# Kernel optimization log

Measured on AMD Instinct MI355X. Metric: run time of the kernel, lower is better.

## Reference

```python
import jax, jax.numpy as jnp
import numpy as np

B, N = 2, 65536
OUT_FEATS = (64, 128, 256)
RES = (64, 32, 16)
EPS = 1e-8


def _grid_sample_border(feat, uv):
    # feat: (B,C,H,W); uv: (B,Np,2) normalized to [-1,1], align_corners=True,
    # bilinear, padding_mode='border' (matches F.grid_sample semantics).
    Bb, C, H, W = feat.shape
    f = jnp.transpose(feat, (0, 2, 3, 1))  # (B,H,W,C)
    ix = jnp.clip((uv[..., 0] + 1.0) * 0.5 * (W - 1), 0.0, W - 1)
    iy = jnp.clip((uv[..., 1] + 1.0) * 0.5 * (H - 1), 0.0, H - 1)
    x0 = jnp.floor(ix); y0 = jnp.floor(iy)
    wx = (ix - x0)[..., None]; wy = (iy - y0)[..., None]
    x0i = x0.astype(jnp.int32); y0i = y0.astype(jnp.int32)
    x1i = jnp.minimum(x0i + 1, W - 1); y1i = jnp.minimum(y0i + 1, H - 1)
    b = jnp.arange(Bb)[:, None]
    v00 = f[b, y0i, x0i]; v01 = f[b, y0i, x1i]
    v10 = f[b, y1i, x0i]; v11 = f[b, y1i, x1i]
    return (v00 * (1 - wx) * (1 - wy) + v01 * wx * (1 - wy)
            + v10 * (1 - wx) * wy + v11 * wx * wy)  # (B,Np,C)


def _projection(img_feat, init_pc, extrinsic, intrinsic):
    homo = jnp.concatenate([init_pc, jnp.ones_like(init_pc[..., :1])], axis=-1)  # (B,N,4)
    P = jnp.einsum('bij,bjk->bik', intrinsic, extrinsic)  # (B,3,4)
    pln = jnp.einsum('bik,bnk->bni', P, homo)  # (B,N,3)
    X, Y, Z = pln[..., 0], pln[..., 1], pln[..., 2]
    uv = jnp.stack([-X / Z, Y / Z], axis=-1)  # sign = -1 since is_srn_proj=False
    return _grid_sample_border(img_feat, uv)


def _adain(pc_feat, img_feat, fcw, fcb):
    mu = jnp.mean(pc_feat, axis=-1, keepdims=True)
    var = jnp.var(pc_feat, axis=-1, ddof=1, keepdims=True)  # torch unbiased var
    pcn = (pc_feat - mu) / jnp.sqrt(var + EPS)
    im_mean = jnp.mean(img_feat, axis=(2, 3))  # (B,C)
    im_var = jnp.var(img_feat.reshape(img_feat.shape[0], img_feat.shape[1], -1), axis=2, ddof=1)
    out = (pcn + im_mean[:, None]) * jnp.sqrt(im_var[:, None] + EPS)
    return out @ fcw + fcb


def setup_inputs() -> dict:
    key = jax.random.key(0)
    ks = iter(jax.random.split(key, 64))
    inp = {}
    inp['init_pc'] = jax.random.uniform(next(ks), (B, N, 3), minval=-1.0, maxval=1.0)
    # extrinsic = [I | t] with t = (0,0,4) plus tiny noise -> Z in ~[3,5], safe division
    ex = jnp.concatenate([jnp.eye(3), jnp.array([[0.0], [0.0], [4.0]])], axis=1)
    inp['extrinsic'] = jnp.broadcast_to(ex, (B, 3, 4)) + 0.01 * jax.random.normal(next(ks), (B, 3, 4))
    intr = jnp.diag(jnp.array([1.2, 1.2, 1.0]))
    inp['intrinsic'] = jnp.broadcast_to(intr, (B, 3, 3)) + 0.01 * jax.random.normal(next(ks), (B, 3, 3))
    for i, (c, r) in enumerate(zip(OUT_FEATS, RES)):
        inp[f'img_feat{i}'] = jax.random.normal(next(ks), (B, c, r, r), dtype=jnp.float32)
    dim = 3
    for i, c in enumerate(OUT_FEATS):
        inp[f'w1_{i}'] = 0.05 * jax.random.normal(next(ks), (dim, c))
        inp[f'b1_{i}'] = jnp.zeros((c,))
        inp[f'w2_{i}'] = 0.05 * jax.random.normal(next(ks), (c, c))
        inp[f'b2_{i}'] = jnp.zeros((c,))
        inp[f'fcw_{i}'] = 0.05 * jax.random.normal(next(ks), (c, c))
        inp[f'fcb_{i}'] = jnp.zeros((c,))
        dim = c
    return inp


def reference(img_feat0, img_feat1, img_feat2, init_pc, extrinsic, intrinsic,
              w1_0, b1_0, w2_0, b2_0, fcw_0, fcb_0,
              w1_1, b1_1, w2_1, b2_1, fcw_1, fcb_1,
              w1_2, b1_2, w2_2, b2_2, fcw_2, fcb_2):
    imgs = [img_feat0, img_feat1, img_feat2]
    blocks = [(w1_0, b1_0, w2_0, b2_0, fcw_0, fcb_0),
              (w1_1, b1_1, w2_1, b2_1, fcw_1, fcb_1),
              (w1_2, b1_2, w2_2, b2_2, fcw_2, fcb_2)]
    pc_feats = []
    feat = init_pc
    encoded = []
    for (w1, b1, w2, b2, _, _) in blocks:  # fixed 3-layer stack
        feat = jax.nn.relu(jax.nn.relu(feat @ w1 + b1) @ w2 + b2)
        encoded.append(feat)
    for pcf, img, (_, _, _, _, fcw, fcb) in zip(encoded, imgs, blocks):
        pc_feats.append(_adain(pcf, img, fcw, fcb))
    for img in imgs:
        pc_feats.append(_projection(img, init_pc, extrinsic, intrinsic))
    pc_feats.append(init_pc)
    return jnp.concatenate(pc_feats, axis=-1)  # (B, N, 2*(64+128+256)+3) = (B,N,899)
```

## Files before the change

### kernel.cpp

```cpp
#include <hip/hip_runtime.h>
#include <hip/hip_bf16.h>

typedef __hip_bfloat16 bf16;
typedef unsigned short u16;
typedef unsigned int u32;
typedef __attribute__((ext_vector_type(8))) short s8b;
typedef __attribute__((ext_vector_type(16))) float f32x16;

#define EPSF 1e-8f

__device__ __align__(16) u16 g_wpack[256000];
__device__ __align__(16) u16 g_fcpack[344064];
__device__ float g_bias[896];
__device__ float g_fcS[896];
__device__ float g_fcC[896];
__device__ float g_T0[2 * 64 * 64 * 64];
__device__ float g_T1[2 * 128 * 32 * 32];
__device__ float g_T2[2 * 256 * 16 * 16];

__device__ __forceinline__ float ldf(const void* p, size_t i, int f32v) {
  return f32v ? ((const float*)p)[i] : __bfloat162float(((const bf16*)p)[i]);
}
template <bool F32>
__device__ __forceinline__ float ld(const void* p, size_t i) {
  if constexpr (F32) return ((const float*)p)[i];
  else return __bfloat162float(((const bf16*)p)[i]);
}
__device__ __forceinline__ void stf(void* p, size_t i, float v, int f32v) {
  if (f32v) ((float*)p)[i] = v;
  else ((bf16*)p)[i] = __float2bfloat16(v);
}
__device__ __forceinline__ int detect_f32(const void* extr) {
  float v = ((const float*)extr)[0];
  return (fabsf(v - 1.0f) < 0.25f) ? 1 : 0;
}

__device__ __forceinline__ void splitbf(float v, u16& h, u16& l) {
  bf16 hb = __float2bfloat16(v);
  float hf = __bfloat162float(hb);
  bf16 lb = __float2bfloat16(v - hf);
  h = __builtin_bit_cast(u16, hb);
  l = __builtin_bit_cast(u16, lb);
}
__device__ __forceinline__ float bfjoin(u16 h, u16 l) {
  return __uint_as_float((u32)h << 16) + __uint_as_float((u32)l << 16);
}

__device__ __forceinline__ u16* xaddr(u16* base, int row, int col) {
  int byte = (row << 9) + (col << 1);
  byte ^= (row & 7) << 4;
  return (u16*)((char*)base + byte);
}
__device__ __forceinline__ const u16* xaddrc(const u16* base, int row, int col) {
  int byte = (row << 9) + (col << 1);
  byte ^= (row & 7) << 4;
  return (const u16*)((const char*)base + byte);
}

__device__ __forceinline__ f32x16 MFMA32(s8b a, s8b b, f32x16 c) {
  return __builtin_amdgcn_mfma_f32_32x32x16_bf16(a, b, c, 0, 0, 0);
}

template <bool F32>
__device__ void stats_body(const void* img0, const void* img1, const void* img2,
                           const void* intr, const void* extr,
                           float* wsf, float* red) {
  int bid = blockIdx.x;
  if (bid >= 896) {
    int b = bid - 896;
    int t = threadIdx.x;
    if (t < 12) {
      int r = t >> 2, c = t & 3;
      float acc = 0.f;
      for (int k = 0; k < 3; ++k)
        acc += ld<F32>(intr, b * 9 + r * 3 + k) * ld<F32>(extr, b * 12 + k * 4 + c);
      wsf[b * 12 + r * 4 + c] = acc;
    }
    return;
  }
  const void* src; size_t base; int HW, outidx;
  if (bid < 128) {
    int b = bid >> 6, c = bid & 63;
    src = img0; base = (size_t)(b * 64 + c) * 4096; HW = 4096;
    outidx = 32 + b * 64 + c;
  } else if (bid < 384) {
    int t = bid - 128; int b = t >> 7, c = t & 127;
    src = img1; base = (size_t)(b * 128 + c) * 1024; HW = 1024;
    outidx = 32 + 128 + b * 128 + c;
  } else {
    int t = bid - 384; int b = t >> 8, c = t & 255;
    src = img2; base = (size_t)(b * 256 + c) * 256; HW = 256;
    outidx = 32 + 384 + b * 256 + c;
  }
  float s1 = 0.f, s2 = 0.f;
  for (int i = threadIdx.x; i < HW; i += 256) {
    float v = ld<F32>(src, base + i);
    s1 += v; s2 += v * v;
  }
  for (int off = 32; off; off >>= 1) {
    s1 += __shfl_xor(s1, off);
    s2 += __shfl_xor(s2, off);
  }
  int wid = threadIdx.x >> 6, lane = threadIdx.x & 63;
  if (lane == 0) { red[wid] = s1; red[4 + wid] = s2; }
  __syncthreads();
  if (threadIdx.x == 0) {
    float S1 = red[0] + red[1] + red[2] + red[3];
    float S2 = red[4] + red[5] + red[6] + red[7];
    float mu = S1 / (float)HW;
    float var = (S2 - (float)HW * mu * mu) / (float)(HW - 1);
    var = fmaxf(var, 0.f);
    wsf[outidx] = mu;
    wsf[outidx + 896] = sqrtf(var + EPSF);
  }
}

__global__ __launch_bounds__(256) void prep1(
    const void* img0, const void* img1, const void* img2,
    const void* intr, const void* extr,
    const void* w1_0, const void* w2_0, const void* w1_1, const void* w2_1,
    const void* w1_2, const void* w2_2,
    const void* b1_0, const void* b2_0, const void* b1_1, const void* b2_1,
    const void* b1_2, const void* b2_2,
    float* wsf) {
  __shared__ float red[8];
  const int f32v = detect_f32(extr);
  int bid = blockIdx.x;
  int tid = threadIdx.x;

  if (bid < 898) {
    if (f32v) stats_body<true>(img0, img1, img2, intr, extr, wsf, red);
    else      stats_body<false>(img0, img1, img2, intr, extr, wsf, red);
    return;
  }
  if (bid < 4482) {
    const void* src; float* dst; int C, R, i0;
    if (bid < 2946)       { src = img0; dst = g_T0; C = 64;  R = 64; i0 = (bid - 898) * 256; }
    else if (bid < 3970)  { src = img1; dst = g_T1; C = 128; R = 32; i0 = (bid - 2946) * 256; }
    else                  { src = img2; dst = g_T2; C = 256; R = 16; i0 = (bid - 3970) * 256; }
    int i = i0 + tid;
    int x = i % R; int t = i / R;
    int y = t % R; t /= R;
    int c = t % C; int b = t / C;
    dst[((size_t)(b * R + y) * R + x) * C + c] = ldf(src, i, f32v);
    return;
  }
  if (bid < 4607) {
    int chunk = (bid - 4482) * 4 + (tid >> 6);
    int lane = tid & 63;
    if (chunk < 500) {
      const int nch[6]   = {4, 16, 32, 64, 128, 256};
      const int cbase[6] = {0, 4, 20, 52, 116, 244};
      const int couts[6] = {64, 64, 128, 128, 256, 256};
      const int kreal[6] = {3, 64, 64, 128, 128, 256};
      const void* wp[6] = {w1_0, w2_0, w1_1, w2_1, w1_2, w2_2};
      int layer = 5;
      for (int s = 0; s < 5; ++s) if (chunk < cbase[s + 1]) { layer = s; break; }
      int ci = chunk - cbase[layer];
      int COUT = couts[layer], KR = kreal[layer];
      int STR = COUT >> 5;
      int ks = ci / (STR * 2);
      int rem = ci % (STR * 2);
      int nt = rem >> 1, split = rem & 1;
      const void* W = wp[layer];
      s8b sv;
#pragma unroll
      for (int j = 0; j < 8; ++j) {
        int k = ks * 16 + 8 * (lane >> 5) + j;
        int c = nt * 32 + (lane & 31);
        float v = (k < KR) ? ldf(W, (size_t)k * COUT + c, f32v) : 0.f;
        u16 h, l; splitbf(v, h, l);
        sv[j] = (short)(split == 0 ? h : l);
      }
      *(s8b*)((char*)g_wpack + (size_t)chunk * 1024 + lane * 16) = sv;
    }
    return;
  }
  {
    int t = (bid - 4607) * 256 + tid;
    if (t < 896) {
      const int off[7] = {0, 64, 128, 256, 384, 640, 896};
      const void* bp[6] = {b1_0, b2_0, b1_1, b2_1, b1_2, b2_2};
      int seg = 0;
      while (seg < 5 && t >= off[seg + 1]) ++seg;
      g_bias[t] = ldf(bp[seg], t - off[seg], f32v);
    }
  }
}

__global__ __launch_bounds__(256) void prep2(
    const void* extr,
    const void* fcw_0, const void* fcw_1, const void* fcw_2,
    const void* fcb_0, const void* fcb_1, const void* fcb_2,
    const float* wsf) {
  const int f32v = detect_f32(extr);
  int bid = blockIdx.x;
  int tid = threadIdx.x;
  if (bid < 168) {
    int chunk = bid * 4 + (tid >> 6);
    int lane = tid & 63;
    int bb = chunk / 336;
    int ci = chunk % 336;
    int C, COUT, loff; const void* W;
    if (ci < 16)      { C = 64;  COUT = 64;  loff = 0;   W = fcw_0; }
    else if (ci < 80) { C = 128; COUT = 128; loff = 128; W = fcw_1; ci -= 16; }
    else              { C = 256; COUT = 256; loff = 384; W = fcw_2; ci -= 80; }
    int STR = COUT >> 5;
    int ks = ci / (STR * 2);
    int rem = ci % (STR * 2);
    int nt = rem >> 1, split = rem & 1;
    const float* sig = wsf + 928 + loff + bb * C;
    s8b sv;
#pragma unroll
    for (int j = 0; j < 8; ++j) {
      int k = ks * 16 + 8 * (lane >> 5) + j;
      int c = nt * 32 + (lane & 31);
      float v = sig[k] * ldf(W, (size_t)k * COUT + c, f32v);
      u16 h, l; splitbf(v, h, l);
      sv[j] = (short)(split == 0 ? h : l);
    }
    *(s8b*)((char*)g_fcpack + (size_t)chunk * 1024 + lane * 16) = sv;
    return;
  }
  {
    int idx = bid - 168;
    if (idx >= 6) return;
    int bb = idx / 3, layer = idx % 3;
    int C, colbase, loff; const void* W; const void* fb;
    if (layer == 0)      { C = 64;  colbase = 0;   loff = 0;   W = fcw_0; fb = fcb_0; }
    else if (layer == 1) { C = 128; colbase = 64;  loff = 128; W = fcw_1; fb = fcb_1; }
    else                 { C = 256; colbase = 192; loff = 384; W = fcw_2; fb = fcb_2; }
    int j = tid;
    if (j >= C) return;
    const float* sig = wsf + 928 + loff + bb * C;
    const float* mean = wsf + 32 + loff + bb * C;
    float S = 0.f, Cv = 0.f;
    for (int c = 0; c < C; ++c) {
      float w = sig[c] * ldf(W, (size_t)c * C + j, f32v);
      S += w;
      Cv += mean[c] * w;
    }
    Cv += ldf(fb, j, f32v);
    g_fcS[bb * 448 + colbase + j] = S;
    g_fcC[bb * 448 + colbase + j] = Cv;
  }
}

template <int KS, int COUT, int NTW, bool HASBIAS>
__device__ __forceinline__ void mm32(
    const u16* Xh_, const u16* Xl_, const char* wlane,
    const float* biasp, int nt0, int lane, f32x16* acc) {
#pragma unroll
  for (int n = 0; n < NTW; ++n) {
    float bv = HASBIAS ? biasp[(nt0 + n) * 32 + (lane & 31)] : 0.f;
#pragma unroll
    for (int q = 0; q < 16; ++q) acc[n][q] = bv;
  }
  const int rowA = lane & 31;
  const int acol = (lane >> 5) * 8;
#pragma unroll
  for (int ks = 0; ks < KS; ++ks) {
    s8b ah = *(const s8b*)xaddrc(Xh_, rowA, ks * 16 + acol);
    s8b al = *(const s8b*)xaddrc(Xl_, rowA, ks * 16 + acol);
#pragma unroll
    for (int n = 0; n < NTW; ++n) {
      const char* ch = wlane + (size_t)((ks * (COUT / 32) + nt0 + n) * 2) * 1024;
      s8b bh = *(const s8b*)(ch);
      s8b bl = *(const s8b*)(ch + 1024);
      acc[n] = MFMA32(ah, bh, acc[n]);
      acc[n] = MFMA32(ah, bl, acc[n]);
      acc[n] = MFMA32(al, bh, acc[n]);
    }
  }
}

template <int COUT>
__device__ __forceinline__ void strip_assign(int wid, int& nt0, int& active) {
  if constexpr (COUT == 64)      { nt0 = (wid & 1);  active = (wid < 2); }
  else if constexpr (COUT == 128){ nt0 = wid;        active = 1; }
  else                           { nt0 = wid * 2;    active = 1; }
}

template <int KS, int COUT>
__device__ __forceinline__ void dense32(u16* Xh_, u16* Xl_,
                                        int wbyte, int bbase, int tid) {
  constexpr int NTW = (COUT == 256) ? 2 : 1;
  int lane = tid & 63, wid = tid >> 6;
  int nt0, active;
  strip_assign<COUT>(wid, nt0, active);
  f32x16 acc[NTW];
  if (active)
    mm32<KS, COUT, NTW, true>(Xh_, Xl_,
        (const char*)g_wpack + wbyte + lane * 16, g_bias + bbase, nt0, lane, acc);
  __syncthreads();
  if (active) {
    int g = lane >> 5;
#pragma unroll
    for (int n = 0; n < NTW; ++n) {
      int col = (nt0 + n) * 32 + (lane & 31);
#pragma unroll
      for (int q = 0; q < 16; ++q) {
        int row = (q & 3) + 8 * (q >> 2) + 4 * g;
        float v = fmaxf(acc[n][q], 0.f);
        u16 h, l; splitbf(v, h, l);
        *xaddr(Xh_, row, col) = h;
        *xaddr(Xl_, row, col) = l;
      }
    }
  }
  __syncthreads();
}

template <int C>
__device__ __forceinline__ void musig(const u16* Xh_, const u16* Xl_,
                                      int lane, float& mu, float& rs) {
  int row = lane & 31;
  int c0 = (lane >> 5) * (C / 2);
  float s1 = 0.f, s2 = 0.f;
#pragma unroll
  for (int k = 0; k < C / 2; k += 8) {
    s8b h = *(const s8b*)xaddrc(Xh_, row, c0 + k);
    s8b l = *(const s8b*)xaddrc(Xl_, row, c0 + k);
#pragma unroll
    for (int i = 0; i < 8; ++i) {
      float f = bfjoin((u16)h[i], (u16)l[i]);
      s1 += f; s2 += f * f;
    }
  }
  s1 += __shfl_xor(s1, 32);
  s2 += __shfl_xor(s2, 32);
  mu = s1 / (float)C;
  float var = (s2 - (float)C * mu * mu) / (float)(C - 1);
  var = fmaxf(var, 0.f);
  rs = 1.0f / sqrtf(var + EPSF);
}

template <int KS, int COUT>
__device__ __forceinline__ void fc32(const u16* Xh_, const u16* Xl_,
    int fcbyte, int scbase, float mu, float rs,
    void* out, u32 R0, int colbase, int f32v, int tid) {
  constexpr int NTW = (COUT == 256) ? 2 : 1;
  int lane = tid & 63, wid = tid >> 6;
  int nt0, active;
  strip_assign<COUT>(wid, nt0, active);
  if (!active) return;
  f32x16 acc[NTW];
  mm32<KS, COUT, NTW, false>(Xh_, Xl_,
      (const char*)g_fcpack + fcbyte + lane * 16, nullptr, nt0, lane, acc);
  float Sv[NTW], Cv[NTW];
  u32 gcol[NTW];
#pragma unroll
  for (int n = 0; n < NTW; ++n) {
    int lc = (nt0 + n) * 32 + (lane & 31);
    Sv[n] = g_fcS[scbase + lc];
    Cv[n] = g_fcC[scbase + lc];
    gcol[n] = colbase + lc;
  }
  int g = lane >> 5;
  if (f32v) {
#pragma unroll
    for (int q = 0; q < 16; ++q) {
      int row = (q & 3) + 8 * (q >> 2) + 4 * g;
      float m = __shfl(mu, row);
      float r = __shfl(rs, row);
      u32 grow = (R0 + row) * 899u;
#pragma unroll
      for (int n = 0; n < NTW; ++n)
        ((float*)out)[grow + gcol[n]] = r * (acc[n][q] - m * Sv[n]) + Cv[n];
    }
  } else {
#pragma unroll
    for (int q = 0; q < 16; ++q) {
      int row = (q & 3) + 8 * (q >> 2) + 4 * g;
      float m = __shfl(mu, row);
      float r = __shfl(rs, row);
      u32 grow = (R0 + row) * 899u;
#pragma unroll
      for (int n = 0; n < NTW; ++n)
        ((bf16*)out)[grow + gcol[n]] =
            __float2bfloat16(r * (acc[n][q] - m * Sv[n]) + Cv[n]);
    }
  }
}

template <int C, int R>
__device__ __forceinline__ void sample(
    const float* T, float u, float v, int b, int lane,
    void* out, u32 obase, int f32v) {
  constexpr int J = C / 64;
  float ix = fminf(fmaxf((u + 1.f) * 0.5f * (float)(R - 1), 0.f), (float)(R - 1));
  float iy = fminf(fmaxf((v + 1.f) * 0.5f * (float)(R - 1), 0.f), (float)(R - 1));
  float x0f = floorf(ix), y0f = floorf(iy);
  float wx = ix - x0f, wy = iy - y0f;
  int x0 = (int)x0f, y0 = (int)y0f;
  int x1 = min(x0 + 1, R - 1), y1 = min(y0 + 1, R - 1);
  float w00 = (1.f - wx) * (1.f - wy), w01 = wx * (1.f - wy);
  float w10 = (1.f - wx) * wy,         w11 = wx * wy;
  const float* T00 = T + (size_t)((b * R + y0) * R + x0) * C;
  const float* T01 = T + (size_t)((b * R + y0) * R + x1) * C;
  const float* T10 = T + (size_t)((b * R + y1) * R + x0) * C;
  const float* T11 = T + (size_t)((b * R + y1) * R + x1) * C;
  float sv[J];
#pragma unroll
  for (int j = 0; j < J; ++j) {
    int c = lane + 64 * j;
    sv[j] = T00[c] * w00 + T01[c] * w01 + T10[c] * w10 + T11[c] * w11;
  }
  if (f32v) {
#pragma unroll
    for (int j = 0; j < J; ++j)
      ((float*)out)[obase + lane + 64 * j] = sv[j];
  } else {
#pragma unroll
    for (int j = 0; j < J; ++j)
      ((bf16*)out)[obase + lane + 64 * j] = __float2bfloat16(sv[j]);
  }
}

__device__ void projection(const void* init_pc, const float* wsf, void* out,
                           u32 R0, int b, int f32v, int tid) {
  int lane = tid & 63, wid = tid >> 6;
  float Pm[12];
#pragma unroll
  for (int i = 0; i < 12; ++i) Pm[i] = wsf[b * 12 + i];
  for (int p = 0; p < 8; ++p) {
    u32 n = R0 + wid * 8 + p;
    float px = ldf(init_pc, (size_t)n * 3 + 0, f32v);
    float py = ldf(init_pc, (size_t)n * 3 + 1, f32v);
    float pz = ldf(init_pc, (size_t)n * 3 + 2, f32v);
    float X = Pm[0] * px + Pm[1] * py + Pm[2] * pz + Pm[3];
    float Y = Pm[4] * px + Pm[5] * py + Pm[6] * pz + Pm[7];
    float Z = Pm[8] * px + Pm[9] * py + Pm[10] * pz + Pm[11];
    float u = -X / Z, vv = Y / Z;
    u32 rowb = n * 899u;
    sample<64, 64>(g_T0, u, vv, b, lane, out, rowb + 448, f32v);
    sample<128, 32>(g_T1, u, vv, b, lane, out, rowb + 512, f32v);
    sample<256, 16>(g_T2, u, vv, b, lane, out, rowb + 640, f32v);
    if (lane < 3) {
      float pv = (lane == 0) ? px : (lane == 1) ? py : pz;
      stf(out, rowb + 896 + lane, pv, f32v);
    }
  }
}

__global__ __launch_bounds__(256, 5) void pce_main(
    const void* init_pc, const void* extr, const float* wsf, void* out) {
  __shared__ u16 Xh[8192];
  __shared__ u16 Xl[8192];
  const int f32v = detect_f32(extr);
  const int tid = threadIdx.x;
  const int lane = tid & 63;
  const u32 R0 = blockIdx.x * 32;
  const int b = (int)(R0 >> 16);

  for (int i = tid; i < 512; i += 256) {
    int r = i >> 4, c = i & 15;
    *xaddr(Xh, r, c) = 0;
    *xaddr(Xl, r, c) = 0;
  }
  __syncthreads();
  if (tid < 96) {
    int r = tid / 3, c = tid % 3;
    float v = ldf(init_pc, (size_t)(R0 + r) * 3 + c, f32v);
    u16 h, l; splitbf(v, h, l);
    *xaddr(Xh, r, c) = h;
    *xaddr(Xl, r, c) = l;
  }
  __syncthreads();

  dense32<1, 64>(Xh, Xl, 0, 0, tid);
  dense32<4, 64>(Xh, Xl, 4096, 64, tid);
  { float mu, rs; musig<64>(Xh, Xl, lane, mu, rs);
    fc32<4, 64>(Xh, Xl, b * 344064 + 0, b * 448 + 0, mu, rs, out, R0, 0, f32v, tid); }

  dense32<4, 128>(Xh, Xl, 20480, 128, tid);
  dense32<8, 128>(Xh, Xl, 53248, 256, tid);
  { float mu, rs; musig<128>(Xh, Xl, lane, mu, rs);
    fc32<8, 128>(Xh, Xl, b * 344064 + 16384, b * 448 + 64, mu, rs, out, R0, 64, f32v, tid); }

  dense32<8, 256>(Xh, Xl, 118784, 384, tid);
  dense32<16, 256>(Xh, Xl, 249856, 640, tid);
  { float mu, rs; musig<256>(Xh, Xl, lane, mu, rs);
    fc32<16, 256>(Xh, Xl, b * 344064 + 81920, b * 448 + 192, mu, rs, out, R0, 192, f32v, tid); }

  projection(init_pc, wsf, out, R0, b, f32v, tid);
}

extern "C" void kernel_launch(void* const* d_in, const int* in_sizes, int n_in,
                              void* d_out, int out_size, void* d_ws, size_t ws_size,
                              hipStream_t stream) {
  const void* init_pc = d_in[0];
  const void* extr    = d_in[1];
  const void* intr    = d_in[2];
  const void* img0    = d_in[3];
  const void* img1    = d_in[4];
  const void* img2    = d_in[5];
  const void* w1_0 = d_in[6],  *b1_0 = d_in[7];
  const void* w2_0 = d_in[8],  *b2_0 = d_in[9];
  const void* fcw_0 = d_in[10], *fcb_0 = d_in[11];
  const void* w1_1 = d_in[12], *b1_1 = d_in[13];
  const void* w2_1 = d_in[14], *b2_1 = d_in[15];
  const void* fcw_1 = d_in[16], *fcb_1 = d_in[17];
  const void* w1_2 = d_in[18], *b1_2 = d_in[19];
  const void* w2_2 = d_in[20], *b2_2 = d_in[21];
  const void* fcw_2 = d_in[22], *fcb_2 = d_in[23];

  float* wsf = (float*)d_ws;

  prep1<<<4611, 256, 0, stream>>>(
      img0, img1, img2, intr, extr,
      w1_0, w2_0, w1_1, w2_1, w1_2, w2_2,
      b1_0, b2_0, b1_1, b2_1, b1_2, b2_2, wsf);
  prep2<<<174, 256, 0, stream>>>(
      extr, fcw_0, fcw_1, fcw_2, fcb_0, fcb_1, fcb_2, wsf);
  pce_main<<<4096, 256, 0, stream>>>(init_pc, extr, wsf, d_out);
}
```

Before: 900.9 us.

## Stage output rows in shared memory for coalesced stores; tile image transpose

The main kernel keeps the three FC accumulators live, then assembles 8 full 899-wide output rows at a time in shared memory (FC results, sampled projections, raw points). It writes them out as contiguous, coalesced non-temporal stores, packing bf16 pairs into 32-bit words. The goal is to replace the scattered strided per-column global writes. The image NHWC transpose in prep1 now goes through a padded shared tile, one block per (batch,row) plane, so both reads and writes are coalesced. The costs are higher register pressure (occupancy hint lowered to 3), extra barriers, and per-element division in the store loop.

Measured after the change: 809.5 us. 1.11x faster.

```diff
diff --git a/kernel.cpp b/kernel.cpp
--- a/kernel.cpp
+++ b/kernel.cpp
@@ -26,10 +26,6 @@
   if constexpr (F32) return ((const float*)p)[i];
   else return __bfloat162float(((const bf16*)p)[i]);
 }
-__device__ __forceinline__ void stf(void* p, size_t i, float v, int f32v) {
-  if (f32v) ((float*)p)[i] = v;
-  else ((bf16*)p)[i] = __float2bfloat16(v);
-}
 __device__ __forceinline__ int detect_f32(const void* extr) {
   float v = ((const float*)extr)[0];
   return (fabsf(v - 1.0f) < 0.25f) ? 1 : 0;
@@ -44,6 +40,9 @@
 }
 __device__ __forceinline__ float bfjoin(u16 h, u16 l) {
   return __uint_as_float((u32)h << 16) + __uint_as_float((u32)l << 16);
+}
+__device__ __forceinline__ u16 f2bfu(float v) {
+  return __builtin_bit_cast(u16, __float2bfloat16(v));
 }
 
 __device__ __forceinline__ u16* xaddr(u16* base, int row, int col) {
@@ -124,6 +123,7 @@
     const void* b1_2, const void* b2_2,
     float* wsf) {
   __shared__ float red[8];
+  __shared__ float tl[4352];
   const int f32v = detect_f32(extr);
   int bid = blockIdx.x;
   int tid = threadIdx.x;
@@ -133,23 +133,28 @@
     else      stats_body<false>(img0, img1, img2, intr, extr, wsf, red);
     return;
   }
-  if (bid < 4482) {
-    const void* src; float* dst; int C, R, i0;
-    if (bid < 2946)       { src = img0; dst = g_T0; C = 64;  R = 64; i0 = (bid - 898) * 256; }
-    else if (bid < 3970)  { src = img1; dst = g_T1; C = 128; R = 32; i0 = (bid - 2946) * 256; }
-    else                  { src = img2; dst = g_T2; C = 256; R = 16; i0 = (bid - 3970) * 256; }
-    int i = i0 + tid;
-    int x = i % R; int t = i / R;
-    int y = t % R; t /= R;
-    int c = t % C; int b = t / C;
-    dst[((size_t)(b * R + y) * R + x) * C + c] = ldf(src, i, f32v);
+  if (bid < 1122) {
+    int pl = bid - 898;
+    const void* src; float* dst; int C, R, rsh, csh, b, y;
+    if (pl < 128)      { src = img0; dst = g_T0; C = 64;  R = 64; rsh = 6; csh = 6; b = pl >> 6; y = pl & 63; }
+    else if (pl < 192) { src = img1; dst = g_T1; C = 128; R = 32; rsh = 5; csh = 7; int q = pl - 128; b = q >> 5; y = q & 31; }
+    else               { src = img2; dst = g_T2; C = 256; R = 16; rsh = 4; csh = 8; int q = pl - 192; b = q >> 4; y = q & 15; }
+    int CR = C * R;
+    for (int i = tid; i < CR; i += 256) {
+      int c = i >> rsh, x = i & (R - 1);
+      tl[c * (R + 1) + x] = ldf(src, ((size_t)(b * C + c) * R + y) * R + x, f32v);
+    }
+    __syncthreads();
+    for (int i = tid; i < CR; i += 256) {
+      int x = i >> csh, c = i & (C - 1);
+      dst[((size_t)(b * R + y) * R + x) * C + c] = tl[c * (R + 1) + x];
+    }
     return;
   }
-  if (bid < 4607) {
-    int chunk = (bid - 4482) * 4 + (tid >> 6);
+  if (bid < 1247) {
+    int chunk = (bid - 1122) * 4 + (tid >> 6);
     int lane = tid & 63;
     if (chunk < 500) {
-      const int nch[6]   = {4, 16, 32, 64, 128, 256};
       const int cbase[6] = {0, 4, 20, 52, 116, 244};
       const int couts[6] = {64, 64, 128, 128, 256, 256};
       const int kreal[6] = {3, 64, 64, 128, 128, 256};
@@ -177,7 +182,7 @@
     return;
   }
   {
-    int t = (bid - 4607) * 256 + tid;
+    int t = (bid - 1247) * 256 + tid;
     if (t < 896) {
       const int off[7] = {0, 64, 128, 256, 384, 640, 896};
       const void* bp[6] = {b1_0, b2_0, b1_1, b2_1, b1_2, b2_2};
@@ -274,20 +279,15 @@
   }
 }
 
-template <int COUT>
-__device__ __forceinline__ void strip_assign(int wid, int& nt0, int& active) {
-  if constexpr (COUT == 64)      { nt0 = (wid & 1);  active = (wid < 2); }
-  else if constexpr (COUT == 128){ nt0 = wid;        active = 1; }
-  else                           { nt0 = wid * 2;    active = 1; }
-}
-
 template <int KS, int COUT>
 __device__ __forceinline__ void dense32(u16* Xh_, u16* Xl_,
                                         int wbyte, int bbase, int tid) {
   constexpr int NTW = (COUT == 256) ? 2 : 1;
   int lane = tid & 63, wid = tid >> 6;
   int nt0, active;
-  strip_assign<COUT>(wid, nt0, active);
+  if constexpr (COUT == 64)      { nt0 = (wid & 1);  active = (wid < 2); }
+  else if constexpr (COUT == 128){ nt0 = wid;        active = 1; }
+  else                           { nt0 = wid * 2;    active = 1; }
   f32x16 acc[NTW];
   if (active)
     mm32<KS, COUT, NTW, true>(Xh_, Xl_,
@@ -335,58 +335,9 @@
   rs = 1.0f / sqrtf(var + EPSF);
 }
 
-template <int KS, int COUT>
-__device__ __forceinline__ void fc32(const u16* Xh_, const u16* Xl_,
-    int fcbyte, int scbase, float mu, float rs,
-    void* out, u32 R0, int colbase, int f32v, int tid) {
-  constexpr int NTW = (COUT == 256) ? 2 : 1;
-  int lane = tid & 63, wid = tid >> 6;
-  int nt0, active;
-  strip_assign<COUT>(wid, nt0, active);
-  if (!active) return;
-  f32x16 acc[NTW];
-  mm32<KS, COUT, NTW, false>(Xh_, Xl_,
-      (const char*)g_fcpack + fcbyte + lane * 16, nullptr, nt0, lane, acc);
-  float Sv[NTW], Cv[NTW];
-  u32 gcol[NTW];
-#pragma unroll
-  for (int n = 0; n < NTW; ++n) {
-    int lc = (nt0 + n) * 32 + (lane & 31);
-    Sv[n] = g_fcS[scbase + lc];
-    Cv[n] = g_fcC[scbase + lc];
-    gcol[n] = colbase + lc;
-  }
-  int g = lane >> 5;
-  if (f32v) {
-#pragma unroll
-    for (int q = 0; q < 16; ++q) {
-      int row = (q & 3) + 8 * (q >> 2) + 4 * g;
-      float m = __shfl(mu, row);
-      float r = __shfl(rs, row);
-      u32 grow = (R0 + row) * 899u;
-#pragma unroll
-      for (int n = 0; n < NTW; ++n)
-        ((float*)out)[grow + gcol[n]] = r * (acc[n][q] - m * Sv[n]) + Cv[n];
-    }
-  } else {
-#pragma unroll
-    for (int q = 0; q < 16; ++q) {
-      int row = (q & 3) + 8 * (q >> 2) + 4 * g;
-      float m = __shfl(mu, row);
-      float r = __shfl(rs, row);
-      u32 grow = (R0 + row) * 899u;
-#pragma unroll
-      for (int n = 0; n < NTW; ++n)
-        ((bf16*)out)[grow + gcol[n]] =
-            __float2bfloat16(r * (acc[n][q] - m * Sv[n]) + Cv[n]);
-    }
-  }
-}
-
 template <int C, int R>
-__device__ __forceinline__ void sample(
-    const float* T, float u, float v, int b, int lane,
-    void* out, u32 obase, int f32v) {
+__device__ __forceinline__ void sample_stg(
+    const float* T, float u, float v, int b, int lane, float* stg) {
   constexpr int J = C / 64;
   float ix = fminf(fmaxf((u + 1.f) * 0.5f * (float)(R - 1), 0.f), (float)(R - 1));
   float iy = fminf(fmaxf((v + 1.f) * 0.5f * (float)(R - 1), 0.f), (float)(R - 1));
@@ -400,56 +351,24 @@
   const float* T01 = T + (size_t)((b * R + y0) * R + x1) * C;
   const float* T10 = T + (size_t)((b * R + y1) * R + x0) * C;
   const float* T11 = T + (size_t)((b * R + y1) * R + x1) * C;
-  float sv[J];
 #pragma unroll
   for (int j = 0; j < J; ++j) {
     int c = lane + 64 * j;
-    sv[j] = T00[c] * w00 + T01[c] * w01 + T10[c] * w10 + T11[c] * w11;
-  }
-  if (f32v) {
-#pragma unroll
-    for (int j = 0; j < J; ++j)
-      ((float*)out)[obase + lane + 64 * j] = sv[j];
-  } else {
-#pragma unroll
-    for (int j = 0; j < J; ++j)
-      ((bf16*)out)[obase + lane + 64 * j] = __float2bfloat16(sv[j]);
-  }
-}
-
-__device__ void projection(const void* init_pc, const float* wsf, void* out,
-                           u32 R0, int b, int f32v, int tid) {
-  int lane = tid & 63, wid = tid >> 6;
-  float Pm[12];
-#pragma unroll
-  for (int i = 0; i < 12; ++i) Pm[i] = wsf[b * 12 + i];
-  for (int p = 0; p < 8; ++p) {
-    u32 n = R0 + wid * 8 + p;
-    float px = ldf(init_pc, (size_t)n * 3 + 0, f32v);
-    float py = ldf(init_pc, (size_t)n * 3 + 1, f32v);
-    float pz = ldf(init_pc, (size_t)n * 3 + 2, f32v);
-    float X = Pm[0] * px + Pm[1] * py + Pm[2] * pz + Pm[3];
-    float Y = Pm[4] * px + Pm[5] * py + Pm[6] * pz + Pm[7];
-    float Z = Pm[8] * px + Pm[9] * py + Pm[10] * pz + Pm[11];
-    float u = -X / Z, vv = Y / Z;
-    u32 rowb = n * 899u;
-    sample<64, 64>(g_T0, u, vv, b, lane, out, rowb + 448, f32v);
-    sample<128, 32>(g_T1, u, vv, b, lane, out, rowb + 512, f32v);
-    sample<256, 16>(g_T2, u, vv, b, lane, out, rowb + 640, f32v);
-    if (lane < 3) {
-      float pv = (lane == 0) ? px : (lane == 1) ? py : pz;
-      stf(out, rowb + 896 + lane, pv, f32v);
-    }
-  }
-}
-
-__global__ __launch_bounds__(256, 5) void pce_main(
+    stg[c] = T00[c] * w00 + T01[c] * w01 + T10[c] * w10 + T11[c] * w11;
+  }
+}
+
+__global__ __launch_bounds__(256, 3) void pce_main(
     const void* init_pc, const void* extr, const float* wsf, void* out) {
-  __shared__ u16 Xh[8192];
-  __shared__ u16 Xl[8192];
+  __shared__ __align__(16) u16 Xsh[16384];
+  u16* Xh = Xsh;
+  u16* Xl = Xsh + 8192;
   const int f32v = detect_f32(extr);
   const int tid = threadIdx.x;
   const int lane = tid & 63;
+  const int wid = tid >> 6;
+  const int hi = lane >> 5;
+  const int colc = lane & 31;
   const u32 R0 = blockIdx.x * 32;
   const int b = (int)(R0 >> 16);
 
@@ -468,22 +387,103 @@
   }
   __syncthreads();
 
+  float mu0, rs0, mu1, rs1, mu2, rs2;
+  f32x16 a0[1], a1[1], a2[2];
+
   dense32<1, 64>(Xh, Xl, 0, 0, tid);
   dense32<4, 64>(Xh, Xl, 4096, 64, tid);
-  { float mu, rs; musig<64>(Xh, Xl, lane, mu, rs);
-    fc32<4, 64>(Xh, Xl, b * 344064 + 0, b * 448 + 0, mu, rs, out, R0, 0, f32v, tid); }
+  musig<64>(Xh, Xl, lane, mu0, rs0);
+  if (wid < 2)
+    mm32<4, 64, 1, false>(Xh, Xl,
+        (const char*)g_fcpack + b * 344064 + 0 + lane * 16, nullptr, wid & 1, lane, a0);
 
   dense32<4, 128>(Xh, Xl, 20480, 128, tid);
   dense32<8, 128>(Xh, Xl, 53248, 256, tid);
-  { float mu, rs; musig<128>(Xh, Xl, lane, mu, rs);
-    fc32<8, 128>(Xh, Xl, b * 344064 + 16384, b * 448 + 64, mu, rs, out, R0, 64, f32v, tid); }
+  musig<128>(Xh, Xl, lane, mu1, rs1);
+  mm32<8, 128, 1, false>(Xh, Xl,
+      (const char*)g_fcpack + b * 344064 + 16384 + lane * 16, nullptr, wid, lane, a1);
 
   dense32<8, 256>(Xh, Xl, 118784, 384, tid);
   dense32<16, 256>(Xh, Xl, 249856, 640, tid);
-  { float mu, rs; musig<256>(Xh, Xl, lane, mu, rs);
-    fc32<16, 256>(Xh, Xl, b * 344064 + 81920, b * 448 + 192, mu, rs, out, R0, 192, f32v, tid); }
-
-  projection(init_pc, wsf, out, R0, b, f32v, tid);
+  musig<256>(Xh, Xl, lane, mu2, rs2);
+  mm32<16, 256, 2, false>(Xh, Xl,
+      (const char*)g_fcpack + b * 344064 + 81920 + lane * 16, nullptr, wid * 2, lane, a2);
+
+  __syncthreads();
+
+  const int scb = b * 448;
+  float S0 = 0.f, C0 = 0.f;
+  if (wid < 2) { S0 = g_fcS[scb + wid * 32 + colc]; C0 = g_fcC[scb + wid * 32 + colc]; }
+  float S1 = g_fcS[scb + 64 + wid * 32 + colc];
+  float C1 = g_fcC[scb + 64 + wid * 32 + colc];
+  float S2a = g_fcS[scb + 192 + wid * 64 + colc];
+  float C2a = g_fcC[scb + 192 + wid * 64 + colc];
+  float S2b = g_fcS[scb + 192 + wid * 64 + 32 + colc];
+  float C2b = g_fcC[scb + 192 + wid * 64 + 32 + colc];
+  float Pm[12];
+#pragma unroll
+  for (int i = 0; i < 12; ++i) Pm[i] = wsf[b * 12 + i];
+
+  float* stg = (float*)Xsh;
+
+#pragma unroll
+  for (int g = 0; g < 4; ++g) {
+#pragma unroll
+    for (int qq = 0; qq < 4; ++qq) {
+      int q = 4 * g + qq;
+      int lr = qq + 4 * hi;
+      int trow = 8 * g + lr;
+      float m0 = __shfl(mu0, trow), r0v = __shfl(rs0, trow);
+      float m1 = __shfl(mu1, trow), r1v = __shfl(rs1, trow);
+      float m2 = __shfl(mu2, trow), r2v = __shfl(rs2, trow);
+      if (wid < 2)
+        stg[lr * 904 + (wid * 32 + colc)] = r0v * (a0[0][q] - m0 * S0) + C0;
+      stg[lr * 904 + 64 + wid * 32 + colc] = r1v * (a1[0][q] - m1 * S1) + C1;
+      stg[lr * 904 + 192 + wid * 64 + colc] = r2v * (a2[0][q] - m2 * S2a) + C2a;
+      stg[lr * 904 + 192 + wid * 64 + 32 + colc] = r2v * (a2[1][q] - m2 * S2b) + C2b;
+    }
+#pragma unroll
+    for (int pp = 0; pp < 2; ++pp) {
+      int lr = wid * 2 + pp;
+      u32 n = R0 + 8 * g + lr;
+      float px = ldf(init_pc, (size_t)n * 3 + 0, f32v);
+      float py = ldf(init_pc, (size_t)n * 3 + 1, f32v);
+      float pz = ldf(init_pc, (size_t)n * 3 + 2, f32v);
+      float X = Pm[0] * px + Pm[1] * py + Pm[2] * pz + Pm[3];
+      float Y = Pm[4] * px + Pm[5] * py + Pm[6] * pz + Pm[7];
+      float Z = Pm[8] * px + Pm[9] * py + Pm[10] * pz + Pm[11];
+      float u = -X / Z, vv = Y / Z;
+      float* srow = stg + lr * 904;
+      sample_stg<64, 64>(g_T0, u, vv, b, lane, srow + 448);
+      sample_stg<128, 32>(g_T1, u, vv, b, lane, srow + 512);
+      sample_stg<256, 16>(g_T2, u, vv, b, lane, srow + 640);
+      if (lane < 3) srow[896 + lane] = (lane == 0) ? px : (lane == 1) ? py : pz;
+    }
+    __syncthreads();
+    u32 base = (R0 + 8 * g) * 899u;
+    if (f32v) {
+      float* op = (float*)out + base;
+      for (int i = tid; i < 7192; i += 256) {
+        u32 r = (u32)i / 899u;
+        u32 c = (u32)i - r * 899u;
+        __builtin_nontemporal_store(stg[r * 904 + c], op + i);
+      }
+    } else {
+      u32* op = (u32*)out + (base >> 1);
+      for (int i = tid; i < 3596; i += 256) {
+        u32 e = (u32)i * 2;
+        u32 r = e / 899u;
+        u32 c = e - r * 899u;
+        float v0 = stg[r * 904 + c];
+        u32 r1 = (c + 1 == 899) ? r + 1 : r;
+        u32 c1 = (c + 1 == 899) ? 0 : c + 1;
+        float v1 = stg[r1 * 904 + c1];
+        u32 pk = (u32)f2bfu(v0) | ((u32)f2bfu(v1) << 16);
+        __builtin_nontemporal_store(pk, op + i);
+      }
+    }
+    __syncthreads();
+  }
 }
 
 extern "C" void kernel_launch(void* const* d_in, const int* in_sizes, int n_in,
@@ -507,7 +507,7 @@
 
   float* wsf = (float*)d_ws;
 
-  prep1<<<4611, 256, 0, stream>>>(
+  prep1<<<1251, 256, 0, stream>>>(
       img0, img1, img2, intr, extr,
       w1_0, w2_0, w1_1, w2_1, w1_2, w2_2,
       b1_0, b2_0, b1_1, b2_1, b1_2, b2_2, wsf);
```
